# Kernel optimization log

Hardware: AMD Instinct MI355X
Metric: run time of the kernel (lower is better)

## Reference

```python
import jax, jax.numpy as jnp
import numpy as np


def _conv3x3(x, w, b):
    # x: [B,C,H,W], w: [O,C,3,3]
    y = jax.lax.conv_general_dilated(x, w, window_strides=(1, 1), padding=((1, 1), (1, 1)),
                                     dimension_numbers=('NCHW', 'OIHW', 'NCHW'))
    return y + b[None, :, None, None]


def _radial_weights(ck, wide):
    # ck: [B, wide, H, W] = |radial core|. Returns softmax-normalized per-pixel
    # kernel weights [B, K*K, H, W] with K = 2*wide - 1 (radially symmetric,
    # linearly interpolated between integer radii, zero outside radius mid).
    mid = wide - 1
    ii, jj = np.meshgrid(np.arange(wide), np.arange(wide), indexing='ij')
    d = np.sqrt((ii - mid) ** 2 + (jj - mid) ** 2)
    low = np.floor(d)
    high = np.ceil(d)
    lo_i = np.clip(low, 0, wide - 1).astype(np.int32)
    hi_i = np.clip(high, 0, wide - 1).astype(np.int32)
    mask = (d <= mid).astype(np.float32)  # strictly-greater-than-mid entries zeroed
    w_hi = ((d - low).astype(np.float32)) * mask
    # torch special-cases low==high -> y_low with weight 1
    w_lo = (np.where(low == high, 1.0, high - d).astype(np.float32)) * mask
    w_lo = jnp.asarray(w_lo)[None, :, :, None, None]
    w_hi = jnp.asarray(w_hi)[None, :, :, None, None]
    quad = w_lo * ck[:, lo_i] + w_hi * ck[:, hi_i]  # [B, wide, wide, H, W]
    # flipcat along both spatial kernel dims -> full K x K symmetric kernel
    sym = np.concatenate([np.arange(wide), np.arange(wide - 2, -1, -1)])
    full = quad[:, sym][:, :, sym]  # [B, K, K, H, W]
    B, K, _, H, W = full.shape
    return jax.nn.softmax(full.reshape(B, K * K, H, W), axis=1)


def _kpn_forward(data_with_est, data, w_first, b_first, w_blk1, b_blk1, w_blk2, b_blk2, w_out, b_out):
    x = _conv3x3(data_with_est, w_first, b_first)
    for i in range(3):  # three ResidualBlock_noBN
        y = jax.nn.relu(_conv3x3(x, w_blk1[i], b_blk1[i]))
        x = x + _conv3x3(y, w_blk2[i], b_blk2[i])
    core = _conv3x3(x, w_out, b_out)  # [B, 35, H, W]

    B, N, H, W = data.shape
    outs = [data]
    off = 0
    for wide in range(2, 9):  # sections [2,3,4,5,6,7,8] -> K in 3,5,...,15
        K = 2 * wide - 1
        ck = jnp.abs(core[:, off:off + wide])
        off += wide
        wts = _radial_weights(ck, wide)  # [B, K*K, H, W]
        r = K // 2
        fp = jnp.pad(data, ((0, 0), (0, 0), (r, r), (r, r)))
        # unfold: K*K shifted views, stacked on a new axis -> [B, N, K*K, H, W]
        stack = jnp.stack([fp[:, :, i:i + H, j:j + W]
                           for i in range(K) for j in range(K)], axis=2)
        pred = jnp.sum(wts[:, None] * stack, axis=2)  # [B, N, H, W]
        outs.append(pred)
    return tuple(outs)


def setup_inputs() -> dict:
    key = jax.random.key(0)
    ks = jax.random.split(key, 8)
    B, N, H, W = 1, 3, 384, 384
    f = lambda k, s: jax.random.normal(k, s, dtype=jnp.float32) * 0.05
    return {
        'data_with_est': jax.random.normal(ks[0], (B, 6, H, W), dtype=jnp.float32),
        'data': jax.random.normal(ks[1], (B, N, H, W), dtype=jnp.float32),
        'w_first': f(ks[2], (64, 6, 3, 3)),
        'b_first': jnp.zeros((64,), jnp.float32),
        'w_blk1': f(ks[3], (3, 64, 64, 3, 3)),
        'b_blk1': jnp.zeros((3, 64), jnp.float32),
        'w_blk2': f(ks[4], (3, 64, 64, 3, 3)),
        'b_blk2': jnp.zeros((3, 64), jnp.float32),
        'w_out': f(ks[5], (35, 64, 3, 3)),
        'b_out': jnp.zeros((35,), jnp.float32),
    }


def reference(data_with_est, data, w_first, b_first, w_blk1, b_blk1, w_blk2, b_blk2, w_out, b_out):
    return _kpn_forward(data_with_est, data, w_first, b_first, w_blk1, b_blk1,
                        w_blk2, b_blk2, w_out, b_out)
```

## Files before the change

### kernel.cpp

```cpp
#include <hip/hip_runtime.h>
#include <hip/hip_bf16.h>
#include <utility>

typedef __attribute__((ext_vector_type(4))) float f32x4;
typedef __attribute__((ext_vector_type(8))) short bf16x8;
typedef __attribute__((ext_vector_type(4))) unsigned short u16x4;
typedef unsigned short u16;

constexpr int HH = 384, WW = 384;
constexpr int AWP = 386;
constexpr int ASTR = AWP * 64;
constexpr int NPIX = HH * WW;
constexpr int NPIX3 = NPIX * 3;
constexpr int DP = 398, DPLANE = DP * DP;
constexpr size_t ACT_BYTES = (size_t)AWP * AWP * 64 * 2;
constexpr int WSW = 72 * 512;
constexpr int WP1N = 12 * 512;

__device__ __forceinline__ u16 f2bf(float f) {
  union { __hip_bfloat16 h; u16 u; } v; v.h = __float2bfloat16(f); return v.u;
}
__device__ __forceinline__ float bf2f(u16 u) {
  union { float f; unsigned int i; } v; v.i = ((unsigned int)u) << 16; return v.f;
}

constexpr int PR_REPACK = 7 * WSW + 448 + WP1N;
constexpr int PR_PADCOPY = PR_REPACK + NPIX3;
constexpr int PR_PAD6 = PR_PADCOPY + NPIX;
constexpr int PR_HALO = PR_PAD6 + 49280 + 3080 + 32844;

__global__ void prep_kern(const float* __restrict__ w1, const float* __restrict__ w2,
                          const float* __restrict__ wo, const float* __restrict__ b1,
                          const float* __restrict__ b2, const float* __restrict__ bo,
                          const float* __restrict__ wf, const float* __restrict__ data,
                          const float* __restrict__ din6,
                          u16* __restrict__ wpack, float* __restrict__ bpack,
                          u16* __restrict__ wp1, float* __restrict__ dpad,
                          u16* __restrict__ in8, u16* __restrict__ A0,
                          u16* __restrict__ A1)
{
  const int gidx = blockIdx.x * 256 + threadIdx.x;
  if (gidx < PR_REPACK) {
    const int idx = gidx;
    constexpr int NW = 7 * WSW;
    if (idx < NW) {
      const int c = idx / WSW;
      const int r = idx % WSW;
      const int iter = r / 512;
      const int lane = (r % 512) / 8;
      const int j = r % 8;
      const int tap = iter >> 3;
      const int ich = (iter >> 2) & 1;
      const int m = iter & 3;
      const int oc = m * 16 + (lane & 15);
      const int ic = ich * 32 + (lane >> 4) * 8 + j;
      float v;
      if (c < 6) {
        const float* s = (c & 1) ? w2 : w1;
        v = s[(((c >> 1) * 64 + oc) * 64 + ic) * 9 + tap];
      } else {
        v = (oc < 35) ? wo[(oc * 64 + ic) * 9 + tap] : 0.f;
      }
      wpack[idx] = f2bf(v);
    } else if (idx < NW + 448) {
      const int t = idx - NW;
      const int c = t / 64, oc = t % 64;
      float v;
      if (c < 6) v = ((c & 1) ? b2 : b1)[(c >> 1) * 64 + oc];
      else v = (oc < 35) ? bo[oc] : 0.f;
      bpack[t] = v;
    } else {
      const int t = idx - NW - 448;
      const int iter = t / 512;
      const int lane = (t % 512) / 8;
      const int j = t % 8;
      const int m = iter & 3;
      const int kb = iter >> 2;
      const int oc = m * 16 + (lane & 15);
      const int k = kb * 32 + (lane >> 4) * 8 + j;
      const int tap = k >> 3, ic = k & 7;
      const float v = (tap < 9 && ic < 6) ? wf[oc * 54 + ic * 9 + tap] : 0.f;
      wp1[t] = f2bf(v);
    }
  } else if (gidx < PR_PADCOPY) {
    const int idx = gidx - PR_REPACK;
    const int c = idx / NPIX, r = idx % NPIX;
    const int y = r / WW, x = r % WW;
    dpad[c * DPLANE + (y + 7) * DP + (x + 7)] = data[idx];
  } else if (gidx < PR_PAD6) {
    const int px = gidx - PR_PADCOPY;
    const int y = px / WW, x = px % WW;
    u16 vals[8];
    #pragma unroll
    for (int ic = 0; ic < 6; ++ic) vals[ic] = f2bf(din6[ic * NPIX + px]);
    vals[6] = 0; vals[7] = 0;
    u16* o = in8 + ((size_t)(y + 1) * AWP + (x + 1)) * 8;
    *(u16x4*)(o) = u16x4{vals[0], vals[1], vals[2], vals[3]};
    *(u16x4*)(o + 4) = u16x4{vals[4], vals[5], vals[6], vals[7]};
  } else if (gidx < PR_HALO) {
    const int idx = gidx - PR_PAD6;
    if (idx < 49280) {
      u16* buf = (idx < 24640) ? A0 : A1;
      const int t = (idx < 24640) ? idx : idx - 24640;
      const int pos = t >> 4, q = t & 15;
      int y, x;
      if (pos < 386) { y = 0; x = pos; }
      else if (pos < 772) { y = 385; x = pos - 386; }
      else if (pos < 1156) { y = pos - 772 + 1; x = 0; }
      else { y = pos - 1156 + 1; x = 385; }
      *(u16x4*)(buf + ((size_t)y * AWP + x) * 64 + q * 4) = u16x4{0, 0, 0, 0};
    } else if (idx < 49280 + 3080) {
      const int t = idx - 49280;
      const int pos = t >> 1, q = t & 1;
      int y, x;
      if (pos < 386) { y = 0; x = pos; }
      else if (pos < 772) { y = 385; x = pos - 386; }
      else if (pos < 1156) { y = pos - 772 + 1; x = 0; }
      else { y = pos - 1156 + 1; x = 385; }
      *(u16x4*)(in8 + ((size_t)y * AWP + x) * 8 + q * 4) = u16x4{0, 0, 0, 0};
    } else {
      const int t = idx - 52360;
      const int c = t / 10948, r = t % 10948;
      int y, x;
      if (r < 2786) { y = r / 398; x = r % 398; }
      else if (r < 5572) { const int rr = r - 2786; y = 391 + rr / 398; x = rr % 398; }
      else { const int rr = r - 5572; y = 7 + rr / 14; const int k = rr % 14; x = (k < 7) ? k : 384 + k; }
      dpad[(size_t)c * DPLANE + (size_t)y * DP + x] = 0.f;
    }
  }
}

__global__ __launch_bounds__(64)
void conv1_mfma(const u16* __restrict__ in8, const u16* __restrict__ wp,
                const float* __restrict__ bias, u16* __restrict__ outb)
{
  const int lane = threadIdx.x;
  const int l15 = lane & 15, g8 = lane >> 4;
  const int bid = blockIdx.x;
  const int sw = (bid & 7) * 288 + (bid >> 3);
  const int y = sw / 6;
  const int x0 = (sw % 6) * 64;

  f32x4 acc[4][4];
  #pragma unroll
  for (int m = 0; m < 4; ++m)
    #pragma unroll
    for (int n = 0; n < 4; ++n)
      acc[m][n] = f32x4{0.f, 0.f, 0.f, 0.f};

  #pragma unroll
  for (int kb = 0; kb < 3; ++kb) {
    const int tap = kb * 4 + g8;
    const int vt = tap < 9 ? tap : 0;
    const int kr = vt / 3, kc = vt % 3;
    const u16* inr = in8 + ((size_t)(y + kr) * AWP + x0 + kc) * 8;
    bf16x8 a[4], b[4];
    #pragma unroll
    for (int m = 0; m < 4; ++m)
      a[m] = *(const bf16x8*)(wp + (kb * 4 + m) * 512 + lane * 8);
    #pragma unroll
    for (int n = 0; n < 4; ++n)
      b[n] = *(const bf16x8*)(inr + (size_t)(n * 16 + l15) * 8);
    #pragma unroll
    for (int m = 0; m < 4; ++m)
      #pragma unroll
      for (int n = 0; n < 4; ++n)
        acc[m][n] = __builtin_amdgcn_mfma_f32_16x16x32_bf16(a[m], b[n], acc[m][n], 0, 0, 0);
  }

  const int oc_lo = g8 * 4;
  #pragma unroll
  for (int m = 0; m < 4; ++m) {
    const int oc0 = m * 16 + oc_lo;
    const f32x4 bv = *(const f32x4*)(bias + oc0);
    #pragma unroll
    for (int n = 0; n < 4; ++n) {
      const int px = x0 + n * 16 + l15;
      const f32x4 v = acc[m][n] + bv;
      u16x4 s;
      #pragma unroll
      for (int j = 0; j < 4; ++j) s[j] = f2bf(v[j]);
      *(u16x4*)(outb + ((size_t)(y + 1) * AWP + (px + 1)) * 64 + oc0) = s;
    }
  }
}

template<int MODE>
__global__ __launch_bounds__(256, 3)
void conv_mfma(const u16* __restrict__ in, const u16* __restrict__ wp,
               const float* __restrict__ bias, u16* __restrict__ outb,
               float* __restrict__ outf)
{
  __shared__ u16 smem[3 * 136 * 64];
  const int lane = threadIdx.x & 63;
  const int wv = threadIdx.x >> 6;
  const int pxh = wv >> 1;
  const int ich = wv & 1;
  const int l15 = lane & 15, g8 = lane >> 4;
  const int bid = blockIdx.x;
  const int sw = (bid & 7) * 144 + (bid >> 3);
  const int y = sw / 3;
  const int x0 = (sw % 3) * 128;

  {
    const int pxl = lane >> 3;
    const int s = lane & 7;
    #pragma unroll
    for (int row = 0; row < 3; ++row) {
      const char* gbase = (const char*)(in + (size_t)(y + row) * ASTR + (size_t)x0 * 64);
      #pragma unroll
      for (int j = 0; j < 17; ++j) {
        if (((row * 17 + j) & 3) == wv) {
          const int px = j * 8 + pxl;
          const char* g = gbase + px * 128 + ((s ^ (px & 7)) << 4);
          __builtin_amdgcn_global_load_lds(
              (__attribute__((address_space(1))) const void*)g,
              (__attribute__((address_space(3))) void*)((char*)smem + row * 17408 + j * 1024),
              16, 0, 0);
        }
      }
    }
  }
  __syncthreads();

  f32x4 acc[4][4];
  #pragma unroll
  for (int m = 0; m < 4; ++m)
    #pragma unroll
    for (int n = 0; n < 4; ++n)
      acc[m][n] = f32x4{0.f, 0.f, 0.f, 0.f};

  const int chunk = ich * 4 + g8;
  #pragma unroll
  for (int tap = 0; tap < 9; ++tap) {
    const int kr = tap / 3, kc = tap % 3;
    const u16* wpi = wp + ((tap * 2 + ich) * 4) * 512 + lane * 8;
    bf16x8 a[4], b[4];
    #pragma unroll
    for (int m = 0; m < 4; ++m)
      a[m] = *(const bf16x8*)(wpi + m * 512);
    #pragma unroll
    for (int n = 0; n < 4; ++n) {
      const int p = pxh * 64 + kc + n * 16 + l15;
      const char* bp = (const char*)smem + kr * 17408 + p * 128 + ((chunk ^ (p & 7)) << 4);
      b[n] = *(const bf16x8*)bp;
    }
    #pragma unroll
    for (int m = 0; m < 4; ++m)
      #pragma unroll
      for (int n = 0; n < 4; ++n)
        acc[m][n] = __builtin_amdgcn_mfma_f32_16x16x32_bf16(a[m], b[n], acc[m][n], 0, 0, 0);
  }

  __syncthreads();
  float* red = (float*)smem;
  if (ich == 1) {
    #pragma unroll
    for (int m = 0; m < 4; ++m)
      #pragma unroll
      for (int n = 0; n < 4; ++n)
        *(f32x4*)(red + pxh * 4096 + (m * 4 + n) * 256 + lane * 4) = acc[m][n];
  }
  __syncthreads();
  if (ich == 1) return;

  const int oc_lo = g8 * 4;
  #pragma unroll
  for (int m = 0; m < 4; ++m) {
    const int oc0 = m * 16 + oc_lo;
    const f32x4 bv = *(const f32x4*)(bias + oc0);
    #pragma unroll
    for (int n = 0; n < 4; ++n) {
      const int px = x0 + pxh * 64 + n * 16 + l15;
      f32x4 v = acc[m][n] + *(const f32x4*)(red + pxh * 4096 + (m * 4 + n) * 256 + lane * 4) + bv;
      if constexpr (MODE == 0) {
        #pragma unroll
        for (int j = 0; j < 4; ++j) v[j] = v[j] > 0.f ? v[j] : 0.f;
      }
      if constexpr (MODE == 1) {
        const u16x4 rr = *(const u16x4*)(outb + ((size_t)(y + 1) * AWP + (px + 1)) * 64 + oc0);
        #pragma unroll
        for (int j = 0; j < 4; ++j) v[j] += bf2f(rr[j]);
      }
      if constexpr (MODE <= 1) {
        u16x4 s;
        #pragma unroll
        for (int j = 0; j < 4; ++j) s[j] = f2bf(v[j]);
        *(u16x4*)(outb + ((size_t)(y + 1) * AWP + (px + 1)) * 64 + oc0) = s;
      } else {
        #pragma unroll
        for (int j = 0; j < 4; ++j) {
          const int oc = oc0 + j;
          if (oc < 35) outf[(size_t)oc * NPIX + (size_t)y * WW + px] = v[j];
        }
      }
    }
  }
}

constexpr int isqrt_(int d2) { int li = 0; while ((li + 1) * (li + 1) <= d2) ++li; return li; }
constexpr double csqrt_(double x) {
  double g = x < 1.0 ? 1.0 : x;
  for (int i = 0; i < 60; ++i) g = 0.5 * (g + x / g);
  return g;
}
constexpr int KOFFS[7] = {0, 2, 5, 9, 14, 20, 27};

template<int SEC0, int NSEC, int CKN, int A, int B, int T>
__device__ __forceinline__ void kpn_sec_one(const float (&g)[3], const float (&ck)[CKN],
                                            float (&s)[NSEC], float (&p)[NSEC][3])
{
  constexpr int WIDE = SEC0 + T + 2;
  if constexpr (A < WIDE && B < WIDE) {
    constexpr int d2 = A * A + B * B;
    constexpr int li = isqrt_(d2);
    constexpr bool exact = (li * li == d2);
    constexpr int hraw = exact ? li : li + 1;
    constexpr float dd = (float)csqrt_((double)d2);
    constexpr float wlo = exact ? 1.0f : ((float)hraw - dd);
    constexpr float whi = exact ? 0.0f : (dd - (float)li);
    constexpr float mult = ((A > 0) ? 2.0f : 1.0f) * ((B > 0) ? 2.0f : 1.0f);
    constexpr int lidx = li < WIDE - 1 ? li : WIDE - 1;
    constexpr int hidx = hraw < WIDE - 1 ? hraw : WIDE - 1;
    constexpr bool msk = d2 <= (WIDE - 1) * (WIDE - 1);
    constexpr int cb = KOFFS[SEC0 + T] - KOFFS[SEC0];
    float e;
    if constexpr (msk) e = __expf(wlo * ck[cb + lidx] + whi * ck[cb + hidx]);
    else e = 1.0f;
    s[T] += mult * e;
    p[T][0] += e * g[0];
    p[T][1] += e * g[1];
    p[T][2] += e * g[2];
  }
}

template<int SEC0, int NSEC, int CKN, int A, int B, int... Ts>
__device__ __forceinline__ void kpn_secs(std::integer_sequence<int, Ts...>,
                                         const float (&g)[3], const float (&ck)[CKN],
                                         float (&s)[NSEC], float (&p)[NSEC][3])
{
  (kpn_sec_one<SEC0, NSEC, CKN, A, B, Ts>(g, ck, s, p), ...);
}

template<int SEC0, int NSEC, int CKN, int WMAX, int C>
__device__ __forceinline__ void kpn_cell(const float* __restrict__ base,
                                         const float (&ck)[CKN],
                                         float (&s)[NSEC], float (&p)[NSEC][3])
{
  constexpr int A = C / WMAX, B = C % WMAX;
  float g[3];
  #pragma unroll
  for (int c = 0; c < 3; ++c) {
    const float* bc = base + c * DPLANE;
    float v = bc[A * DP + B];
    if constexpr (B > 0) v += bc[A * DP - B];
    if constexpr (A > 0) v += bc[-A * DP + B];
    if constexpr (A > 0 && B > 0) v += bc[-A * DP - B];
    g[c] = v;
  }
  kpn_secs<SEC0, NSEC, CKN, A, B>(std::make_integer_sequence<int, NSEC>{}, g, ck, s, p);
}

template<int SEC0, int NSEC, int CKN, int WMAX, int... Cs>
__device__ __forceinline__ void kpn_cells(std::integer_sequence<int, Cs...>,
                                          const float* __restrict__ base,
                                          const float (&ck)[CKN],
                                          float (&s)[NSEC], float (&p)[NSEC][3])
{
  (kpn_cell<SEC0, NSEC, CKN, WMAX, Cs>(base, ck, s, p), ...);
}

template<int SEC0, int NSEC>
__device__ __forceinline__ void kpn_grp_body(const float* __restrict__ corep,
                                             const float* __restrict__ dpad,
                                             float* __restrict__ out)
{
  constexpr int WMAX = SEC0 + NSEC + 1;
  constexpr int CK0 = KOFFS[SEC0];
  constexpr int CKN = KOFFS[SEC0 + NSEC - 1] + (SEC0 + NSEC + 1) - CK0;

  const int bid = blockIdx.x;
  const int sw = (bid & 7) * 72 + (bid >> 3);
  const int px = sw * 256 + threadIdx.x;
  const int y = px / WW, x = px % WW;
  const float* base = dpad + (size_t)(y + 7) * DP + (x + 7);

  float ck[CKN];
  #pragma unroll
  for (int i = 0; i < CKN; ++i) ck[i] = fabsf(corep[(size_t)(CK0 + i) * NPIX + px]);

  float s[NSEC], p[NSEC][3];
  #pragma unroll
  for (int k = 0; k < NSEC; ++k) { s[k] = 0.f; p[k][0] = 0.f; p[k][1] = 0.f; p[k][2] = 0.f; }

  kpn_cells<SEC0, NSEC, CKN, WMAX>(std::make_integer_sequence<int, WMAX * WMAX>{},
                                   base, ck, s, p);

  #pragma unroll
  for (int t = 0; t < NSEC; ++t) {
    const float inv = 1.f / s[t];
    float* o = out + (size_t)(SEC0 + t + 1) * NPIX3 + px;
    o[0] = p[t][0] * inv;
    o[NPIX] = p[t][1] * inv;
    o[2 * NPIX] = p[t][2] * inv;
  }
}

__global__ __launch_bounds__(256, 2)
void kpn_fused7(const float* __restrict__ corep, const float* __restrict__ dpad,
                float* __restrict__ out)
{
  kpn_grp_body<0, 7>(corep, dpad, out);
}

extern "C" void kernel_launch(void* const* d_in, const int* in_sizes, int n_in,
                              void* d_out, int out_size, void* d_ws, size_t ws_size,
                              hipStream_t stream)
{
  const float* d_est   = (const float*)d_in[0];
  const float* data    = (const float*)d_in[1];
  const float* w_first = (const float*)d_in[2];
  const float* b_first = (const float*)d_in[3];
  const float* w_blk1  = (const float*)d_in[4];
  const float* b_blk1  = (const float*)d_in[5];
  const float* w_blk2  = (const float*)d_in[6];
  const float* b_blk2  = (const float*)d_in[7];
  const float* w_out   = (const float*)d_in[8];
  const float* b_out   = (const float*)d_in[9];

  char* ws = (char*)d_ws;
  const size_t OFF_A1    = ACT_BYTES;
  const size_t OFF_CORE  = 2 * ACT_BYTES;
  const size_t OFF_DPAD  = OFF_CORE + (size_t)35 * NPIX * 4;
  const size_t OFF_WPACK = OFF_DPAD + (size_t)3 * DPLANE * 4;
  const size_t OFF_BPACK = OFF_WPACK + (size_t)7 * WSW * 2;
  const size_t OFF_WP1   = OFF_BPACK + 448 * 4;
  const size_t OFF_IN8   = OFF_WP1 + (size_t)WP1N * 2;

  u16*   A0    = (u16*)(ws);
  u16*   A1    = (u16*)(ws + OFF_A1);
  float* corep = (float*)(ws + OFF_CORE);
  float* dpad  = (float*)(ws + OFF_DPAD);
  u16*   wpack = (u16*)(ws + OFF_WPACK);
  float* bpack = (float*)(ws + OFF_BPACK);
  u16*   wp1   = (u16*)(ws + OFF_WP1);
  u16*   in8   = (u16*)(ws + OFF_IN8);

  hipMemcpyAsync(d_out, data, (size_t)NPIX3 * 4, hipMemcpyDeviceToDevice, stream);

  prep_kern<<<3671, 256, 0, stream>>>(w_blk1, w_blk2, w_out, b_blk1, b_blk2, b_out,
                                      w_first, data, d_est,
                                      wpack, bpack, wp1, dpad, in8, A0, A1);
  conv1_mfma<<<2304, 64, 0, stream>>>(in8, wp1, b_first, A0);

  for (int i = 0; i < 3; ++i) {
    conv_mfma<0><<<1152, 256, 0, stream>>>(A0, wpack + (size_t)(2 * i) * WSW,
                                           bpack + (2 * i) * 64, A1, nullptr);
    conv_mfma<1><<<1152, 256, 0, stream>>>(A1, wpack + (size_t)(2 * i + 1) * WSW,
                                           bpack + (2 * i + 1) * 64, A0, nullptr);
  }
  conv_mfma<2><<<1152, 256, 0, stream>>>(A0, wpack + (size_t)6 * WSW,
                                         bpack + 6 * 64, nullptr, corep);

  kpn_fused7<<<576, 256, 0, stream>>>(corep, dpad, (float*)d_out);
}
```

Before: 183.1 us.

## Vectorize KPN row loads, trim output conv MFMA rows, relax launch bounds

The KPN fused kernel now loads each kernel row as four unaligned float4 vectors per channel, folds the mirrored rows and columns in registers, and then runs all column cells from registers instead of issuing up to four scalar loads per cell. The output conv (MODE 2, 35 channels) computes only 3 of the 4 16-channel MFMA row tiles, skipping work on padding channels. The launch_bounds occupancy hint of 2 is removed from the KPN kernel, so the compiler may use more registers at lower occupancy. The intent is to cut load instruction count and wasted MFMA work; the risks are unaligned vector loads and register pressure.

```diff
diff --git a/kernel.cpp b/kernel.cpp
--- a/kernel.cpp
+++ b/kernel.cpp
@@ -3,6 +3,7 @@
 #include <utility>
 
 typedef __attribute__((ext_vector_type(4))) float f32x4;
+typedef float f32x4u __attribute__((ext_vector_type(4), aligned(4)));
 typedef __attribute__((ext_vector_type(8))) short bf16x8;
 typedef __attribute__((ext_vector_type(4))) unsigned short u16x4;
 typedef unsigned short u16;
@@ -191,6 +192,7 @@
                const float* __restrict__ bias, u16* __restrict__ outb,
                float* __restrict__ outf)
 {
+  constexpr int MM = (MODE == 2) ? 3 : 4;
   __shared__ u16 smem[3 * 136 * 64];
   const int lane = threadIdx.x & 63;
   const int wv = threadIdx.x >> 6;
@@ -223,9 +225,9 @@
   }
   __syncthreads();
 
-  f32x4 acc[4][4];
-  #pragma unroll
-  for (int m = 0; m < 4; ++m)
+  f32x4 acc[MM][4];
+  #pragma unroll
+  for (int m = 0; m < MM; ++m)
     #pragma unroll
     for (int n = 0; n < 4; ++n)
       acc[m][n] = f32x4{0.f, 0.f, 0.f, 0.f};
@@ -235,9 +237,9 @@
   for (int tap = 0; tap < 9; ++tap) {
     const int kr = tap / 3, kc = tap % 3;
     const u16* wpi = wp + ((tap * 2 + ich) * 4) * 512 + lane * 8;
-    bf16x8 a[4], b[4];
-    #pragma unroll
-    for (int m = 0; m < 4; ++m)
+    bf16x8 a[MM], b[4];
+    #pragma unroll
+    for (int m = 0; m < MM; ++m)
       a[m] = *(const bf16x8*)(wpi + m * 512);
     #pragma unroll
     for (int n = 0; n < 4; ++n) {
@@ -246,7 +248,7 @@
       b[n] = *(const bf16x8*)bp;
     }
     #pragma unroll
-    for (int m = 0; m < 4; ++m)
+    for (int m = 0; m < MM; ++m)
       #pragma unroll
       for (int n = 0; n < 4; ++n)
         acc[m][n] = __builtin_amdgcn_mfma_f32_16x16x32_bf16(a[m], b[n], acc[m][n], 0, 0, 0);
@@ -256,7 +258,7 @@
   float* red = (float*)smem;
   if (ich == 1) {
     #pragma unroll
-    for (int m = 0; m < 4; ++m)
+    for (int m = 0; m < MM; ++m)
       #pragma unroll
       for (int n = 0; n < 4; ++n)
         *(f32x4*)(red + pxh * 4096 + (m * 4 + n) * 256 + lane * 4) = acc[m][n];
@@ -266,7 +268,7 @@
 
   const int oc_lo = g8 * 4;
   #pragma unroll
-  for (int m = 0; m < 4; ++m) {
+  for (int m = 0; m < MM; ++m) {
     const int oc0 = m * 16 + oc_lo;
     const f32x4 bv = *(const f32x4*)(bias + oc0);
     #pragma unroll
@@ -342,32 +344,61 @@
   (kpn_sec_one<SEC0, NSEC, CKN, A, B, Ts>(g, ck, s, p), ...);
 }
 
-template<int SEC0, int NSEC, int CKN, int WMAX, int C>
-__device__ __forceinline__ void kpn_cell(const float* __restrict__ base,
+template<int SEC0, int NSEC, int CKN, int A, int B>
+__device__ __forceinline__ void kpn_bcol(const float (&rf)[3][8], const float (&ck)[CKN],
+                                         float (&s)[NSEC], float (&p)[NSEC][3])
+{
+  const float g[3] = {rf[0][B], rf[1][B], rf[2][B]};
+  kpn_secs<SEC0, NSEC, CKN, A, B>(std::make_integer_sequence<int, NSEC>{}, g, ck, s, p);
+}
+
+template<int SEC0, int NSEC, int CKN, int A, int... Bs>
+__device__ __forceinline__ void kpn_bcols(std::integer_sequence<int, Bs...>,
+                                          const float (&rf)[3][8], const float (&ck)[CKN],
+                                          float (&s)[NSEC], float (&p)[NSEC][3])
+{
+  (kpn_bcol<SEC0, NSEC, CKN, A, Bs>(rf, ck, s, p), ...);
+}
+
+template<int SEC0, int NSEC, int CKN, int WMAX, int A>
+__device__ __forceinline__ void kpn_arow(const float* __restrict__ base,
                                          const float (&ck)[CKN],
                                          float (&s)[NSEC], float (&p)[NSEC][3])
 {
-  constexpr int A = C / WMAX, B = C % WMAX;
-  float g[3];
+  float rf[3][8];
   #pragma unroll
   for (int c = 0; c < 3; ++c) {
     const float* bc = base + c * DPLANE;
-    float v = bc[A * DP + B];
-    if constexpr (B > 0) v += bc[A * DP - B];
-    if constexpr (A > 0) v += bc[-A * DP + B];
-    if constexpr (A > 0 && B > 0) v += bc[-A * DP - B];
-    g[c] = v;
-  }
-  kpn_secs<SEC0, NSEC, CKN, A, B>(std::make_integer_sequence<int, NSEC>{}, g, ck, s, p);
-}
-
-template<int SEC0, int NSEC, int CKN, int WMAX, int... Cs>
-__device__ __forceinline__ void kpn_cells(std::integer_sequence<int, Cs...>,
+    f32x4u v[4];
+    #pragma unroll
+    for (int q = 0; q < 4; ++q)
+      v[q] = *(const f32x4u*)(bc + A * DP - 7 + q * 4);
+    if constexpr (A > 0) {
+      #pragma unroll
+      for (int q = 0; q < 4; ++q) {
+        const f32x4u w = *(const f32x4u*)(bc - A * DP - 7 + q * 4);
+        v[q] += w;
+      }
+    }
+    rf[c][0] = v[1][3];
+    rf[c][1] = v[2][0] + v[1][2];
+    rf[c][2] = v[2][1] + v[1][1];
+    rf[c][3] = v[2][2] + v[1][0];
+    rf[c][4] = v[2][3] + v[0][3];
+    rf[c][5] = v[3][0] + v[0][2];
+    rf[c][6] = v[3][1] + v[0][1];
+    rf[c][7] = v[3][2] + v[0][0];
+  }
+  kpn_bcols<SEC0, NSEC, CKN, A>(std::make_integer_sequence<int, WMAX>{}, rf, ck, s, p);
+}
+
+template<int SEC0, int NSEC, int CKN, int WMAX, int... As>
+__device__ __forceinline__ void kpn_arows(std::integer_sequence<int, As...>,
                                           const float* __restrict__ base,
                                           const float (&ck)[CKN],
                                           float (&s)[NSEC], float (&p)[NSEC][3])
 {
-  (kpn_cell<SEC0, NSEC, CKN, WMAX, Cs>(base, ck, s, p), ...);
+  (kpn_arow<SEC0, NSEC, CKN, WMAX, As>(base, ck, s, p), ...);
 }
 
 template<int SEC0, int NSEC>
@@ -393,7 +424,7 @@
   #pragma unroll
   for (int k = 0; k < NSEC; ++k) { s[k] = 0.f; p[k][0] = 0.f; p[k][1] = 0.f; p[k][2] = 0.f; }
 
-  kpn_cells<SEC0, NSEC, CKN, WMAX>(std::make_integer_sequence<int, WMAX * WMAX>{},
+  kpn_arows<SEC0, NSEC, CKN, WMAX>(std::make_integer_sequence<int, WMAX>{},
                                    base, ck, s, p);
 
   #pragma unroll
@@ -406,7 +437,7 @@
   }
 }
 
-__global__ __launch_bounds__(256, 2)
+__global__ __launch_bounds__(256)
 void kpn_fused7(const float* __restrict__ corep, const float* __restrict__ dpad,
                 float* __restrict__ out)
 {
```

After: 181.9 us, median of 3. Within noise of the previous version (-0.7%).
